# Kernel tuning notes

Measured on AMD Instinct MI355X. Metric: run time of the kernel, lower is better.

Reference implementation:

```python
import jax, jax.numpy as jnp
import numpy as np

N_NODES = 100000


def setup_inputs() -> dict:
    key = jax.random.key(0)
    ks = jax.random.split(key, 7)
    n, d, c, e = N_NODES, 256, 128, 3200000
    features = jax.random.normal(ks[0], (n, d), dtype=jnp.float32)
    adj_row = jax.random.randint(ks[1], (e,), 0, n, dtype=jnp.int32)
    adj_col = jax.random.randint(ks[2], (e,), 0, n, dtype=jnp.int32)
    adj_vals = jax.random.uniform(ks[3], (e,), dtype=jnp.float32)
    kernel = jax.random.normal(ks[4], (d, c), dtype=jnp.float32) * (1.0 / np.sqrt(d))
    bias = jax.random.normal(ks[5], (c,), dtype=jnp.float32) * 0.01
    skip_weight = jax.random.normal(ks[6], (c,), dtype=jnp.float32)
    return {"features": features, "adj_row": adj_row, "adj_col": adj_col,
            "adj_vals": adj_vals, "kernel": kernel, "bias": bias,
            "skip_weight": skip_weight}


def reference(features, adj_row, adj_col, adj_vals, kernel, bias, skip_weight):
    # h = X @ W  : [n, c]
    h = features @ kernel
    # SpMM: out[r] += A[r, c] * h[c] over edges (COO)
    msgs = adj_vals[:, None] * h[adj_col]            # [e, c]
    agg = jax.ops.segment_sum(msgs, adj_row, num_segments=N_NODES)  # [n, c]
    out = h * skip_weight + agg                      # skip-connection scale + aggregation
    out = out + bias
    return jax.nn.selu(out)
```

## Files before the change

### kernel.cpp

```cpp
#include <hip/hip_runtime.h>
#include <math.h>

#define N_NODES 100000
#define D 256
#define C 128
#define N_EDGES 3200000
#define ELL_W 80
#define N_PASS 2
#define ROWS_PER_PASS (N_NODES / N_PASS)

typedef __attribute__((ext_vector_type(8))) short bf16x8;
typedef __attribute__((ext_vector_type(4))) float f32x4;
typedef __attribute__((ext_vector_type(4))) unsigned int uint4v;

__device__ __forceinline__ unsigned short f2bf(float f) {
  const unsigned int u = __float_as_uint(f);
  return (unsigned short)((u + 0x7fffu + ((u >> 16) & 1u)) >> 16);
}
__device__ __forceinline__ unsigned int pack_bf(float lo, float hi) {
  return (unsigned int)f2bf(lo) | ((unsigned int)f2bf(hi) << 16);
}
__device__ __forceinline__ float bflo(unsigned int u) {
  return __uint_as_float(u << 16);
}
__device__ __forceinline__ float bfhi(unsigned int u) {
  return __uint_as_float(u & 0xffff0000u);
}
__device__ __forceinline__ float selu1(float x) {
  const float scale = 1.0507009873554804934193349852946f;
  const float alpha = 1.6732632423543772848170429916717f;
  return x > 0.f ? scale * x : scale * alpha * (__expf(x) - 1.f);
}
__device__ __forceinline__ unsigned int pack_rec(int col, float val) {
  return ((unsigned int)col << 15) | ((unsigned int)f2bf(val) & 0x7fffu);
}
__device__ __forceinline__ int rec_col(unsigned int r) { return (int)(r >> 15); }
__device__ __forceinline__ float rec_val(unsigned int r) {
  return __uint_as_float((r & 0x7fffu) << 16);
}
__device__ __forceinline__ bf16x8 packA_nt(const float* p) {
  const f32x4 a0 = __builtin_nontemporal_load(reinterpret_cast<const f32x4*>(p));
  const f32x4 a1 =
      __builtin_nontemporal_load(reinterpret_cast<const f32x4*>(p) + 1);
  union {
    unsigned int u[4];
    bf16x8 v;
  } af;
  af.u[0] = pack_bf(a0[0], a0[1]);
  af.u[1] = pack_bf(a0[2], a0[3]);
  af.u[2] = pack_bf(a1[0], a1[1]);
  af.u[3] = pack_bf(a1[2], a1[3]);
  return af.v;
}

__global__ __launch_bounds__(256) void prep(const float* __restrict__ W,
                                            unsigned short* __restrict__ WT,
                                            int* __restrict__ cnt) {
  const int t = blockIdx.x * blockDim.x + threadIdx.x;
  const int n = t >> 8;
  const int k = t & 255;
  WT[t] = f2bf(W[k * C + n]);
  for (int i = t; i < N_NODES; i += gridDim.x * blockDim.x) cnt[i] = 0;
}

__global__ __launch_bounds__(256) void gemm_scatter(
    const float* __restrict__ X, const unsigned short* __restrict__ WT,
    unsigned short* __restrict__ h2, const int* __restrict__ row,
    const int* __restrict__ col, const float* __restrict__ vals,
    int* __restrict__ cnt, unsigned int* __restrict__ ell) {
  const int bid = blockIdx.x;
  const int tid = threadIdx.x;
  if (bid % 5 == 0) {
    const int wid = (bid / 5) * 4 + (tid >> 6);
    if (wid >= N_NODES / 32) return;
    const int lane = tid & 63;
    const int row0 = wid * 32;
    const int r = lane & 15;
    const int kg = lane >> 4;

    f32x4 acc[2][8];
#pragma unroll
    for (int g = 0; g < 2; ++g)
#pragma unroll
      for (int f = 0; f < 8; ++f) acc[g][f] = (f32x4){0.f, 0.f, 0.f, 0.f};

    const float* arow0 = X + (size_t)(row0 + r) * D + kg * 8;
    const float* arow1 = arow0 + 16 * D;
    for (int k0 = 0; k0 < D; k0 += 32) {
      const bf16x8 a0 = packA_nt(arow0 + k0);
      const bf16x8 a1 = packA_nt(arow1 + k0);
#pragma unroll
      for (int f = 0; f < 8; ++f) {
        const bf16x8 bf = *reinterpret_cast<const bf16x8*>(
            WT + (size_t)(f * 16 + r) * D + k0 + kg * 8);
        acc[0][f] =
            __builtin_amdgcn_mfma_f32_16x16x32_bf16(a0, bf, acc[0][f], 0, 0, 0);
        acc[1][f] =
            __builtin_amdgcn_mfma_f32_16x16x32_bf16(a1, bf, acc[1][f], 0, 0, 0);
      }
    }
#pragma unroll
    for (int g = 0; g < 2; ++g)
#pragma unroll
      for (int f = 0; f < 8; ++f)
#pragma unroll
        for (int j = 0; j < 4; ++j)
          h2[(size_t)(row0 + g * 16 + kg * 4 + j) * C + f * 16 + r] =
              f2bf(acc[g][f][j]);
  } else {
    const int sbid = bid - bid / 5 - 1;
    if (sbid >= N_EDGES / 1024) return;
    const int t = sbid * 256 + tid;
    const int T = N_EDGES / 4;
    const int e0 = t, e1 = t + T, e2 = t + 2 * T, e3 = t + 3 * T;
#pragma unroll
    for (int p = 0; p < N_PASS; ++p) {
      const int lo = p * ROWS_PER_PASS;
      const int hi = lo + ROWS_PER_PASS;
      const int r0 = row[e0];
      const int r1 = row[e1];
      const int r2 = row[e2];
      const int r3 = row[e3];
      if (r0 >= lo && r0 < hi) {
        const int s = atomicAdd(&cnt[r0], 1);
        if (s < ELL_W)
          ell[(size_t)r0 * ELL_W + s] = pack_rec(col[e0], vals[e0]);
      }
      if (r1 >= lo && r1 < hi) {
        const int s = atomicAdd(&cnt[r1], 1);
        if (s < ELL_W)
          ell[(size_t)r1 * ELL_W + s] = pack_rec(col[e1], vals[e1]);
      }
      if (r2 >= lo && r2 < hi) {
        const int s = atomicAdd(&cnt[r2], 1);
        if (s < ELL_W)
          ell[(size_t)r2 * ELL_W + s] = pack_rec(col[e2], vals[e2]);
      }
      if (r3 >= lo && r3 < hi) {
        const int s = atomicAdd(&cnt[r3], 1);
        if (s < ELL_W)
          ell[(size_t)r3 * ELL_W + s] = pack_rec(col[e3], vals[e3]);
      }
    }
  }
}

__global__ __launch_bounds__(256) void ell_gather_selu(
    const int* __restrict__ cnt, const unsigned int* __restrict__ ell,
    const unsigned int* __restrict__ h2u, const float* __restrict__ skip,
    const float* __restrict__ bias, float* __restrict__ out) {
  const int r = (blockIdx.x * blockDim.x + threadIdx.x) >> 6;
  const int lane = threadIdx.x & 63;
  if (r >= N_NODES) return;
  int len = cnt[r];
  len = len < ELL_W ? len : ELL_W;
  const unsigned int* rec = ell + (size_t)r * ELL_W;
  float ax = 0.f, ay = 0.f;
  int j = 0;
  for (; j + 7 < len; j += 8) {
    const uint4v pa =
        __builtin_nontemporal_load(reinterpret_cast<const uint4v*>(rec + j));
    const uint4v pb =
        __builtin_nontemporal_load(reinterpret_cast<const uint4v*>(rec + j + 4));
    const unsigned int u0 = h2u[(size_t)rec_col(pa.x) * 64 + lane];
    const unsigned int u1 = h2u[(size_t)rec_col(pa.y) * 64 + lane];
    const unsigned int u2 = h2u[(size_t)rec_col(pa.z) * 64 + lane];
    const unsigned int u3 = h2u[(size_t)rec_col(pa.w) * 64 + lane];
    const unsigned int u4 = h2u[(size_t)rec_col(pb.x) * 64 + lane];
    const unsigned int u5 = h2u[(size_t)rec_col(pb.y) * 64 + lane];
    const unsigned int u6 = h2u[(size_t)rec_col(pb.z) * 64 + lane];
    const unsigned int u7 = h2u[(size_t)rec_col(pb.w) * 64 + lane];
    ax = fmaf(rec_val(pa.x), bflo(u0), ax);
    ay = fmaf(rec_val(pa.x), bfhi(u0), ay);
    ax = fmaf(rec_val(pa.y), bflo(u1), ax);
    ay = fmaf(rec_val(pa.y), bfhi(u1), ay);
    ax = fmaf(rec_val(pa.z), bflo(u2), ax);
    ay = fmaf(rec_val(pa.z), bfhi(u2), ay);
    ax = fmaf(rec_val(pa.w), bflo(u3), ax);
    ay = fmaf(rec_val(pa.w), bfhi(u3), ay);
    ax = fmaf(rec_val(pb.x), bflo(u4), ax);
    ay = fmaf(rec_val(pb.x), bfhi(u4), ay);
    ax = fmaf(rec_val(pb.y), bflo(u5), ax);
    ay = fmaf(rec_val(pb.y), bfhi(u5), ay);
    ax = fmaf(rec_val(pb.z), bflo(u6), ax);
    ay = fmaf(rec_val(pb.z), bfhi(u6), ay);
    ax = fmaf(rec_val(pb.w), bflo(u7), ax);
    ay = fmaf(rec_val(pb.w), bfhi(u7), ay);
  }
  for (; j + 3 < len; j += 4) {
    const uint4v pa =
        __builtin_nontemporal_load(reinterpret_cast<const uint4v*>(rec + j));
    const unsigned int u0 = h2u[(size_t)rec_col(pa.x) * 64 + lane];
    const unsigned int u1 = h2u[(size_t)rec_col(pa.y) * 64 + lane];
    const unsigned int u2 = h2u[(size_t)rec_col(pa.z) * 64 + lane];
    const unsigned int u3 = h2u[(size_t)rec_col(pa.w) * 64 + lane];
    ax = fmaf(rec_val(pa.x), bflo(u0), ax);
    ay = fmaf(rec_val(pa.x), bfhi(u0), ay);
    ax = fmaf(rec_val(pa.y), bflo(u1), ax);
    ay = fmaf(rec_val(pa.y), bfhi(u1), ay);
    ax = fmaf(rec_val(pa.z), bflo(u2), ax);
    ay = fmaf(rec_val(pa.z), bfhi(u2), ay);
    ax = fmaf(rec_val(pa.w), bflo(u3), ax);
    ay = fmaf(rec_val(pa.w), bfhi(u3), ay);
  }
  for (; j < len; ++j) {
    const unsigned int a = rec[j];
    const float va = rec_val(a);
    const unsigned int u = h2u[(size_t)rec_col(a) * 64 + lane];
    ax = fmaf(va, bflo(u), ax);
    ay = fmaf(va, bfhi(u), ay);
  }
  const unsigned int hr = h2u[(size_t)r * 64 + lane];
  const float2 sk = *reinterpret_cast<const float2*>(skip + lane * 2);
  const float2 bi = *reinterpret_cast<const float2*>(bias + lane * 2);
  const float ox = selu1(fmaf(bflo(hr), sk.x, ax) + bi.x);
  const float oy = selu1(fmaf(bfhi(hr), sk.y, ay) + bi.y);
  *reinterpret_cast<float2*>(out + (size_t)r * C + lane * 2) =
      make_float2(ox, oy);
}

extern "C" void kernel_launch(void* const* d_in, const int* in_sizes, int n_in,
                              void* d_out, int out_size, void* d_ws,
                              size_t ws_size, hipStream_t stream) {
  const float* features = (const float*)d_in[0];
  const int* adj_row = (const int*)d_in[1];
  const int* adj_col = (const int*)d_in[2];
  const float* adj_vals = (const float*)d_in[3];
  const float* W = (const float*)d_in[4];
  const float* bias = (const float*)d_in[5];
  const float* skip = (const float*)d_in[6];
  float* out = (float*)d_out;

  char* ws = (char*)d_ws;
  const size_t SZ_H2 = (size_t)N_NODES * C * 2;
  const size_t OFF_ELL = (SZ_H2 + 255) & ~(size_t)255;
  const size_t SZ_ELL = (size_t)N_NODES * ELL_W * 4;
  const size_t OFF_CNT = OFF_ELL + SZ_ELL;
  const size_t OFF_WT = (OFF_CNT + (size_t)N_NODES * 4 + 255) & ~(size_t)255;
  const size_t NEEDED = OFF_WT + (size_t)D * C * 2;

  if (ws_size < NEEDED) return;

  unsigned short* h2 = (unsigned short*)ws;
  unsigned int* ell = (unsigned int*)(ws + OFF_ELL);
  int* cnt = (int*)(ws + OFF_CNT);
  unsigned short* WT = (unsigned short*)(ws + OFF_WT);

  prep<<<(D * C) / 256, 256, 0, stream>>>(W, WT, cnt);

  gemm_scatter<<<3910, 256, 0, stream>>>(features, WT, h2, adj_row, adj_col,
                                         adj_vals, cnt, ell);

  ell_gather_selu<<<(N_NODES * 64 + 255) / 256, 256, 0, stream>>>(
      cnt, ell, (const unsigned int*)h2, skip, bias, out);
}
```

Measured before the change: 302.0 us.

## Replicate ELL bucket counters per XCD to keep scatter atomics XCD-local

Replaces the two-pass row-range ELL build with per-XCD replicated count arrays and small per-XCD ELL buckets (width 16), plus a shared overflow bucket, selected by reading the hardware XCC id. The aim is to keep atomics and writes local to each die's L2 instead of contending across XCDs, and to drop the second pass over the row array. The gather kernel now walks eight short segments plus overflow per row. This adds a memset of nine count arrays, a much larger workspace, and more fragmented, less vectorized gather loops.

```diff
diff --git a/kernel.cpp b/kernel.cpp
--- a/kernel.cpp
+++ b/kernel.cpp
@@ -5,9 +5,9 @@
 #define D 256
 #define C 128
 #define N_EDGES 3200000
-#define ELL_W 80
-#define N_PASS 2
-#define ROWS_PER_PASS (N_NODES / N_PASS)
+#define REP_W 16
+#define OVF_W 64
+#define NXCD 8
 
 typedef __attribute__((ext_vector_type(8))) short bf16x8;
 typedef __attribute__((ext_vector_type(4))) float f32x4;
@@ -54,20 +54,19 @@
 }
 
 __global__ __launch_bounds__(256) void prep(const float* __restrict__ W,
-                                            unsigned short* __restrict__ WT,
-                                            int* __restrict__ cnt) {
+                                            unsigned short* __restrict__ WT) {
   const int t = blockIdx.x * blockDim.x + threadIdx.x;
   const int n = t >> 8;
   const int k = t & 255;
   WT[t] = f2bf(W[k * C + n]);
-  for (int i = t; i < N_NODES; i += gridDim.x * blockDim.x) cnt[i] = 0;
 }
 
 __global__ __launch_bounds__(256) void gemm_scatter(
     const float* __restrict__ X, const unsigned short* __restrict__ WT,
     unsigned short* __restrict__ h2, const int* __restrict__ row,
     const int* __restrict__ col, const float* __restrict__ vals,
-    int* __restrict__ cnt, unsigned int* __restrict__ ell) {
+    int* __restrict__ cnt, unsigned int* __restrict__ rep,
+    int* __restrict__ ocnt, unsigned int* __restrict__ oell) {
   const int bid = blockIdx.x;
   const int tid = threadIdx.x;
   if (bid % 5 == 0) {
@@ -110,106 +109,83 @@
   } else {
     const int sbid = bid - bid / 5 - 1;
     if (sbid >= N_EDGES / 1024) return;
+    int xcc;
+    asm volatile("s_getreg_b32 %0, hwreg(HW_REG_XCC_ID)" : "=s"(xcc));
+    xcc &= (NXCD - 1);
+    int* mycnt = cnt + (size_t)xcc * N_NODES;
+    unsigned int* myell = rep + (size_t)xcc * N_NODES * REP_W;
+
     const int t = sbid * 256 + tid;
     const int T = N_EDGES / 4;
-    const int e0 = t, e1 = t + T, e2 = t + 2 * T, e3 = t + 3 * T;
-#pragma unroll
-    for (int p = 0; p < N_PASS; ++p) {
-      const int lo = p * ROWS_PER_PASS;
-      const int hi = lo + ROWS_PER_PASS;
-      const int r0 = row[e0];
-      const int r1 = row[e1];
-      const int r2 = row[e2];
-      const int r3 = row[e3];
-      if (r0 >= lo && r0 < hi) {
-        const int s = atomicAdd(&cnt[r0], 1);
-        if (s < ELL_W)
-          ell[(size_t)r0 * ELL_W + s] = pack_rec(col[e0], vals[e0]);
-      }
-      if (r1 >= lo && r1 < hi) {
-        const int s = atomicAdd(&cnt[r1], 1);
-        if (s < ELL_W)
-          ell[(size_t)r1 * ELL_W + s] = pack_rec(col[e1], vals[e1]);
-      }
-      if (r2 >= lo && r2 < hi) {
-        const int s = atomicAdd(&cnt[r2], 1);
-        if (s < ELL_W)
-          ell[(size_t)r2 * ELL_W + s] = pack_rec(col[e2], vals[e2]);
-      }
-      if (r3 >= lo && r3 < hi) {
-        const int s = atomicAdd(&cnt[r3], 1);
-        if (s < ELL_W)
-          ell[(size_t)r3 * ELL_W + s] = pack_rec(col[e3], vals[e3]);
+#pragma unroll
+    for (int q = 0; q < 4; ++q) {
+      const int e = t + q * T;
+      const int r = __builtin_nontemporal_load(row + e);
+      const int c = __builtin_nontemporal_load(col + e);
+      const float v = __builtin_nontemporal_load(vals + e);
+      const unsigned int pr = pack_rec(c, v);
+      const int s = atomicAdd(&mycnt[r], 1);
+      if (s < REP_W) {
+        myell[(size_t)r * REP_W + s] = pr;
+      } else {
+        const int s2 = atomicAdd(&ocnt[r], 1);
+        if (s2 < OVF_W) oell[(size_t)r * OVF_W + s2] = pr;
       }
     }
   }
 }
 
+__device__ __forceinline__ void seg4(const unsigned int* __restrict__ rec,
+                                     int len, const unsigned int* __restrict__ h2u,
+                                     int lane, float& ax, float& ay) {
+  int j = 0;
+  for (; j + 3 < len; j += 4) {
+    const uint4v p =
+        __builtin_nontemporal_load(reinterpret_cast<const uint4v*>(rec + j));
+    const unsigned int u0 = h2u[(size_t)rec_col(p.x) * 64 + lane];
+    const unsigned int u1 = h2u[(size_t)rec_col(p.y) * 64 + lane];
+    const unsigned int u2 = h2u[(size_t)rec_col(p.z) * 64 + lane];
+    const unsigned int u3 = h2u[(size_t)rec_col(p.w) * 64 + lane];
+    ax = fmaf(rec_val(p.x), bflo(u0), ax);
+    ay = fmaf(rec_val(p.x), bfhi(u0), ay);
+    ax = fmaf(rec_val(p.y), bflo(u1), ax);
+    ay = fmaf(rec_val(p.y), bfhi(u1), ay);
+    ax = fmaf(rec_val(p.z), bflo(u2), ax);
+    ay = fmaf(rec_val(p.z), bfhi(u2), ay);
+    ax = fmaf(rec_val(p.w), bflo(u3), ax);
+    ay = fmaf(rec_val(p.w), bfhi(u3), ay);
+  }
+  for (; j < len; ++j) {
+    const unsigned int a = rec[j];
+    const unsigned int u = h2u[(size_t)rec_col(a) * 64 + lane];
+    ax = fmaf(rec_val(a), bflo(u), ax);
+    ay = fmaf(rec_val(a), bfhi(u), ay);
+  }
+}
+
 __global__ __launch_bounds__(256) void ell_gather_selu(
-    const int* __restrict__ cnt, const unsigned int* __restrict__ ell,
+    const int* __restrict__ cnt, const unsigned int* __restrict__ rep,
+    const int* __restrict__ ocnt, const unsigned int* __restrict__ oell,
     const unsigned int* __restrict__ h2u, const float* __restrict__ skip,
     const float* __restrict__ bias, float* __restrict__ out) {
   const int r = (blockIdx.x * blockDim.x + threadIdx.x) >> 6;
   const int lane = threadIdx.x & 63;
   if (r >= N_NODES) return;
-  int len = cnt[r];
-  len = len < ELL_W ? len : ELL_W;
-  const unsigned int* rec = ell + (size_t)r * ELL_W;
   float ax = 0.f, ay = 0.f;
-  int j = 0;
-  for (; j + 7 < len; j += 8) {
-    const uint4v pa =
-        __builtin_nontemporal_load(reinterpret_cast<const uint4v*>(rec + j));
-    const uint4v pb =
-        __builtin_nontemporal_load(reinterpret_cast<const uint4v*>(rec + j + 4));
-    const unsigned int u0 = h2u[(size_t)rec_col(pa.x) * 64 + lane];
-    const unsigned int u1 = h2u[(size_t)rec_col(pa.y) * 64 + lane];
-    const unsigned int u2 = h2u[(size_t)rec_col(pa.z) * 64 + lane];
-    const unsigned int u3 = h2u[(size_t)rec_col(pa.w) * 64 + lane];
-    const unsigned int u4 = h2u[(size_t)rec_col(pb.x) * 64 + lane];
-    const unsigned int u5 = h2u[(size_t)rec_col(pb.y) * 64 + lane];
-    const unsigned int u6 = h2u[(size_t)rec_col(pb.z) * 64 + lane];
-    const unsigned int u7 = h2u[(size_t)rec_col(pb.w) * 64 + lane];
-    ax = fmaf(rec_val(pa.x), bflo(u0), ax);
-    ay = fmaf(rec_val(pa.x), bfhi(u0), ay);
-    ax = fmaf(rec_val(pa.y), bflo(u1), ax);
-    ay = fmaf(rec_val(pa.y), bfhi(u1), ay);
-    ax = fmaf(rec_val(pa.z), bflo(u2), ax);
-    ay = fmaf(rec_val(pa.z), bfhi(u2), ay);
-    ax = fmaf(rec_val(pa.w), bflo(u3), ax);
-    ay = fmaf(rec_val(pa.w), bfhi(u3), ay);
-    ax = fmaf(rec_val(pb.x), bflo(u4), ax);
-    ay = fmaf(rec_val(pb.x), bfhi(u4), ay);
-    ax = fmaf(rec_val(pb.y), bflo(u5), ax);
-    ay = fmaf(rec_val(pb.y), bfhi(u5), ay);
-    ax = fmaf(rec_val(pb.z), bflo(u6), ax);
-    ay = fmaf(rec_val(pb.z), bfhi(u6), ay);
-    ax = fmaf(rec_val(pb.w), bflo(u7), ax);
-    ay = fmaf(rec_val(pb.w), bfhi(u7), ay);
-  }
-  for (; j + 3 < len; j += 4) {
-    const uint4v pa =
-        __builtin_nontemporal_load(reinterpret_cast<const uint4v*>(rec + j));
-    const unsigned int u0 = h2u[(size_t)rec_col(pa.x) * 64 + lane];
-    const unsigned int u1 = h2u[(size_t)rec_col(pa.y) * 64 + lane];
-    const unsigned int u2 = h2u[(size_t)rec_col(pa.z) * 64 + lane];
-    const unsigned int u3 = h2u[(size_t)rec_col(pa.w) * 64 + lane];
-    ax = fmaf(rec_val(pa.x), bflo(u0), ax);
-    ay = fmaf(rec_val(pa.x), bfhi(u0), ay);
-    ax = fmaf(rec_val(pa.y), bflo(u1), ax);
-    ay = fmaf(rec_val(pa.y), bfhi(u1), ay);
-    ax = fmaf(rec_val(pa.z), bflo(u2), ax);
-    ay = fmaf(rec_val(pa.z), bfhi(u2), ay);
-    ax = fmaf(rec_val(pa.w), bflo(u3), ax);
-    ay = fmaf(rec_val(pa.w), bfhi(u3), ay);
-  }
-  for (; j < len; ++j) {
-    const unsigned int a = rec[j];
-    const float va = rec_val(a);
-    const unsigned int u = h2u[(size_t)rec_col(a) * 64 + lane];
-    ax = fmaf(va, bflo(u), ax);
-    ay = fmaf(va, bfhi(u), ay);
-  }
+  int lens[NXCD];
+#pragma unroll
+  for (int x = 0; x < NXCD; ++x) {
+    int l = cnt[(size_t)x * N_NODES + r];
+    lens[x] = l < REP_W ? l : REP_W;
+  }
+#pragma unroll
+  for (int x = 0; x < NXCD; ++x) {
+    seg4(rep + ((size_t)x * N_NODES + r) * REP_W, lens[x], h2u, lane, ax, ay);
+  }
+  int ol = ocnt[r];
+  ol = ol < OVF_W ? ol : OVF_W;
+  if (ol > 0) seg4(oell + (size_t)r * OVF_W, ol, h2u, lane, ax, ay);
+
   const unsigned int hr = h2u[(size_t)r * 64 + lane];
   const float2 sk = *reinterpret_cast<const float2*>(skip + lane * 2);
   const float2 bi = *reinterpret_cast<const float2*>(bias + lane * 2);
@@ -233,24 +209,30 @@
 
   char* ws = (char*)d_ws;
   const size_t SZ_H2 = (size_t)N_NODES * C * 2;
-  const size_t OFF_ELL = (SZ_H2 + 255) & ~(size_t)255;
-  const size_t SZ_ELL = (size_t)N_NODES * ELL_W * 4;
-  const size_t OFF_CNT = OFF_ELL + SZ_ELL;
-  const size_t OFF_WT = (OFF_CNT + (size_t)N_NODES * 4 + 255) & ~(size_t)255;
+  const size_t OFF_REP = (SZ_H2 + 255) & ~(size_t)255;
+  const size_t SZ_REP = (size_t)NXCD * N_NODES * REP_W * 4;
+  const size_t OFF_OELL = OFF_REP + SZ_REP;
+  const size_t SZ_OELL = (size_t)N_NODES * OVF_W * 4;
+  const size_t OFF_CNT = OFF_OELL + SZ_OELL;
+  const size_t SZ_CNT = (size_t)(NXCD + 1) * N_NODES * 4;
+  const size_t OFF_WT = (OFF_CNT + SZ_CNT + 255) & ~(size_t)255;
   const size_t NEEDED = OFF_WT + (size_t)D * C * 2;
 
   if (ws_size < NEEDED) return;
 
   unsigned short* h2 = (unsigned short*)ws;
-  unsigned int* ell = (unsigned int*)(ws + OFF_ELL);
+  unsigned int* rep = (unsigned int*)(ws + OFF_REP);
+  unsigned int* oell = (unsigned int*)(ws + OFF_OELL);
   int* cnt = (int*)(ws + OFF_CNT);
+  int* ocnt = cnt + (size_t)NXCD * N_NODES;
   unsigned short* WT = (unsigned short*)(ws + OFF_WT);
 
-  prep<<<(D * C) / 256, 256, 0, stream>>>(W, WT, cnt);
+  prep<<<(D * C) / 256, 256, 0, stream>>>(W, WT);
+  hipMemsetAsync(cnt, 0, SZ_CNT, stream);
 
   gemm_scatter<<<3910, 256, 0, stream>>>(features, WT, h2, adj_row, adj_col,
-                                         adj_vals, cnt, ell);
+                                         adj_vals, cnt, rep, ocnt, oell);
 
   ell_gather_selu<<<(N_NODES * 64 + 255) / 256, 256, 0, stream>>>(
-      cnt, ell, (const unsigned int*)h2, skip, bias, out);
-}
+      cnt, rep, ocnt, oell, (const unsigned int*)h2, skip, bias, out);
+}
```

Measured after the change: 412.5 us. 1.37x slower.
